# Optimization experiments

Hardware: AMD Instinct MI355X
Metric: run time of the kernel (lower is better)

## Reference

```python
import jax, jax.numpy as jnp
import numpy as np

N, E, D, SD = 50000, 800000, 64, 7

def _lin_init(key, fan_in, shape):
    b = 1.0 / np.sqrt(fan_in)
    return jax.random.uniform(key, shape, minval=-b, maxval=b, dtype=jnp.float32)

def setup_inputs() -> dict:
    key = jax.random.key(0)
    ks = jax.random.split(key, 16)
    edge_index = jax.random.randint(ks[0], (2, E), 0, N, dtype=jnp.int64)
    h = jax.random.normal(ks[1], (N, D), dtype=jnp.float32)
    return {
        "edge_index": edge_index,
        "h": h,
        "W_att": _lin_init(ks[2], D, (D, D)),        # stored [in,out]
        "phi_att_w": _lin_init(ks[3], D, (D, D)),
        "phi_att_b": _lin_init(ks[4], D, (D,)),
        "W_p": _lin_init(ks[5], D, (D, D)),
        "W_pp": _lin_init(ks[6], D, (D, D)),
        "f_def_w": _lin_init(ks[7], D, (D, 1)),
        "f_def_b": _lin_init(ks[8], D, (1,)),
        "W_self_w": _lin_init(ks[9], D, (D, D)),
        "W_self_b": _lin_init(ks[10], D, (D,)),
        "W_A_w": _lin_init(ks[11], D, (D, D)),
        "W_A_b": _lin_init(ks[12], D, (D,)),
        "W_str_w": _lin_init(ks[13], SD - 1, (SD - 1, D)),
        "W_str_b": _lin_init(ks[14], SD - 1, (D,)),
        "ln_g": jnp.ones((D,), jnp.float32),
        "ln_b": jnp.zeros((D,), jnp.float32),
    }

def reference(edge_index, h, W_att, phi_att_w, phi_att_b, W_p, W_pp,
              f_def_w, f_def_b, W_self_w, W_self_b, W_A_w, W_A_b,
              W_str_w, W_str_b, ln_g, ln_b):
    gamma, delta = 1.0, 0.5
    n = h.shape[0]
    src, tgt = edge_index[0], edge_index[1]
    H = h  # in_dim == hidden_dim -> embed is None
    s_feat = h[:, :SD - 1]                      # [N, 6]
    h_src, h_tgt = H[src], H[tgt]               # [E, D] gathers
    # attention-like scatter softmax over incoming edges of tgt
    score = jnp.sum(h_tgt * (h_src @ W_att), axis=-1) \
          + jnp.sum(s_feat[src] * s_feat[tgt], axis=-1)   # [E]
    alpha_num = jnp.exp(score)
    alpha_den = jax.ops.segment_sum(alpha_num, tgt, num_segments=n)
    alpha = alpha_num / (alpha_den[tgt] + 1e-9)
    # pairing / defense term (rev_src=tgt, rev_tgt=src => h_att=H[src], h_def=H[tgt])
    pair = jnp.sum((h_src @ W_p) * (h_tgt @ W_pp), axis=-1)  # [E]
    beta_num = jnp.exp(pair)
    beta_den = jax.ops.segment_sum(beta_num, src, num_segments=n)
    beta = beta_num / (beta_den[src] + 1e-9)
    psi = (h_tgt @ f_def_w)[:, 0] + f_def_b[0]                # [E]
    sum_term = jax.ops.segment_sum(beta * jnp.exp(-psi), src, num_segments=n)
    d = -jnp.log(sum_term + 1e-8)
    rho = jax.nn.sigmoid(gamma * (d - delta))                 # [N]
    rho_edge = rho[src]
    # message + scatter-sum aggregation
    msg = alpha[:, None] * (h_src @ phi_att_w + phi_att_b) * (1.0 - rho_edge)[:, None]
    m_att = jax.ops.segment_sum(msg, tgt, num_segments=n)     # [N, D]
    out = (H @ W_self_w + W_self_b) + (m_att @ W_A_w + W_A_b) \
        + (s_feat @ W_str_w + W_str_b)
    out = jax.nn.relu(out) + H                                # residual
    mu = jnp.mean(out, axis=-1, keepdims=True)
    var = jnp.mean((out - mu) ** 2, axis=-1, keepdims=True)
    out = (out - mu) / jnp.sqrt(var + 1e-5) * ln_g + ln_b     # LayerNorm
    return out
```

## Files before the change

kernel.cpp:

```cpp
#include <hip/hip_runtime.h>
#include <math.h>

#define D 64
#define NB 256
#define SCAN_NB 256

typedef _Float16 hf;
typedef _Float16 hf2 __attribute__((ext_vector_type(2)));

__device__ inline float fdot2f(hf2 a, hf2 b, float c) {
#if __has_builtin(__builtin_amdgcn_fdot2)
    return __builtin_amdgcn_fdot2(a, b, c, false);
#else
    return (float)a[0] * (float)b[0] + (float)a[1] * (float)b[1] + c;
#endif
}

__global__ __launch_bounds__(512) void node_pre_kernel(
    const float* __restrict__ h,
    const float* __restrict__ W_att,
    const float* __restrict__ W_p,
    const float* __restrict__ W_pp,
    const float* __restrict__ phi_w,
    const float* __restrict__ phi_b,
    const float* __restrict__ fdef_w,
    const float* __restrict__ fdef_b,
    hf* __restrict__ AW16,
    hf* __restrict__ P16,
    hf* __restrict__ PP16,
    float* __restrict__ enpsi,
    int nNodes)
{
    __shared__ hf2 sW2[4][32][D];
    __shared__ hf  hall[32][D];
    __shared__ float sPhib[D];
    __shared__ float sFdef[D];

    const int tid = threadIdx.x;
    const float* Wm[4] = { W_att, W_p, W_pp, phi_w };
    for (int idx = tid; idx < 4 * 32 * D; idx += 512) {
        const int m  = idx >> 11;
        const int k2 = (idx >> 6) & 31;
        const int j  = idx & 63;
        sW2[m][k2][j] = hf2{(hf)Wm[m][(2 * k2) * D + j], (hf)Wm[m][(2 * k2 + 1) * D + j]};
    }
    if (tid < D) { sPhib[tid] = phi_b[tid]; sFdef[tid] = fdef_w[tid]; }
    __syncthreads();
    const float fb = fdef_b[0];

    const int n0 = blockIdx.x * 32;
    {
        const int base = tid * 4;
        const int ln = base >> 6;
        const int col = base & 63;
        const int n = n0 + ln;
        float ps = 0.f;
        if (n < nNodes) {
            const float4 v = *(const float4*)(h + (size_t)n * D + col);
            hall[ln][col]     = (hf)v.x;
            hall[ln][col + 1] = (hf)v.y;
            hall[ln][col + 2] = (hf)v.z;
            hall[ln][col + 3] = (hf)v.w;
            ps = v.x * sFdef[col] + v.y * sFdef[col + 1]
               + v.z * sFdef[col + 2] + v.w * sFdef[col + 3];
        }
        #pragma unroll
        for (int off = 8; off >= 1; off >>= 1) ps += __shfl_xor(ps, off, 64);
        if ((tid & 15) == 0 && n < nNodes) enpsi[n] = __expf(-(ps + fb));
    }
    __syncthreads();

    const int g = tid >> 6;
    const int j = tid & 63;
    const int ln0 = 4 * g;

    float acc[4][4];
    #pragma unroll
    for (int m = 0; m < 4; ++m) {
        acc[m][0] = 0.f; acc[m][1] = 0.f; acc[m][2] = 0.f; acc[m][3] = sPhib[j];
    }
    const hf2* hr0 = (const hf2*)hall[ln0 + 0];
    const hf2* hr1 = (const hf2*)hall[ln0 + 1];
    const hf2* hr2 = (const hf2*)hall[ln0 + 2];
    const hf2* hr3 = (const hf2*)hall[ln0 + 3];

    #pragma unroll 8
    for (int k2 = 0; k2 < 32; ++k2) {
        const hf2 w0 = sW2[0][k2][j];
        const hf2 w1 = sW2[1][k2][j];
        const hf2 w2 = sW2[2][k2][j];
        const hf2 w3 = sW2[3][k2][j];
        const hf2 h0 = hr0[k2];
        const hf2 h1 = hr1[k2];
        const hf2 h2 = hr2[k2];
        const hf2 h3 = hr3[k2];
        acc[0][0] = fdot2f(w0, h0, acc[0][0]);
        acc[0][1] = fdot2f(w1, h0, acc[0][1]);
        acc[0][2] = fdot2f(w2, h0, acc[0][2]);
        acc[0][3] = fdot2f(w3, h0, acc[0][3]);
        acc[1][0] = fdot2f(w0, h1, acc[1][0]);
        acc[1][1] = fdot2f(w1, h1, acc[1][1]);
        acc[1][2] = fdot2f(w2, h1, acc[1][2]);
        acc[1][3] = fdot2f(w3, h1, acc[1][3]);
        acc[2][0] = fdot2f(w0, h2, acc[2][0]);
        acc[2][1] = fdot2f(w1, h2, acc[2][1]);
        acc[2][2] = fdot2f(w2, h2, acc[2][2]);
        acc[2][3] = fdot2f(w3, h2, acc[2][3]);
        acc[3][0] = fdot2f(w0, h3, acc[3][0]);
        acc[3][1] = fdot2f(w1, h3, acc[3][1]);
        acc[3][2] = fdot2f(w2, h3, acc[3][2]);
        acc[3][3] = fdot2f(w3, h3, acc[3][3]);
    }

    #pragma unroll
    for (int m = 0; m < 4; ++m) {
        const int n = n0 + ln0 + m;
        if (n < nNodes) {
            float a = acc[m][0];
            if (j < 6) a += (float)hall[ln0 + m][j];
            const size_t base = (size_t)n * D + j;
            *(hf2*)(AW16 + ((size_t)n << 7) + 2 * j) = hf2{(hf)a, (hf)acc[m][3]};
            P16[base]  = (hf)acc[m][1];
            PP16[base] = (hf)acc[m][2];
        }
    }
}

__global__ __launch_bounds__(256) void bucket_hist_kernel(
    const int* __restrict__ tgtI, const int* __restrict__ srcI,
    int* __restrict__ ghist_t, int* __restrict__ ghist_s,
    int nBkt, int nEdges)
{
    __shared__ int hist[2048];
    const int dir = blockIdx.x / NB;
    const int b = blockIdx.x % NB;
    const int* keys = dir ? srcI : tgtI;
    int* gh = dir ? ghist_s : ghist_t;
    const int tid = threadIdx.x;
    for (int d = tid; d < nBkt; d += 256) hist[d] = 0;
    __syncthreads();
    const int C = (nEdges + NB - 1) / NB;
    const int beg = b * C;
    const int end = min(beg + C, nEdges);
    for (int e = beg + tid; e < end; e += 256)
        atomicAdd(&hist[keys[e] >> 5], 1);
    __syncthreads();
    for (int d = tid; d < nBkt; d += 256)
        gh[(size_t)d * NB + b] = hist[d];
}

__global__ __launch_bounds__(256) void scan_partial_kernel(
    const int* __restrict__ in_t, const int* __restrict__ in_s,
    int* __restrict__ bsum, int L)
{
    const int pass = blockIdx.x >> 8;
    const int b = blockIdx.x & (SCAN_NB - 1);
    const int* in = pass ? in_s : in_t;
    const int C = (L + SCAN_NB - 1) / SCAN_NB;
    const int K = (C + 255) / 256;
    const int base = b * C;
    const int lim = min(base + C, L);
    const int tbeg = base + threadIdx.x * K;
    const int tend = min(tbeg + K, lim);
    int tsum = 0;
    for (int i = tbeg; i < tend; ++i) tsum += in[i];
    __shared__ int red[256];
    red[threadIdx.x] = tsum;
    __syncthreads();
    for (int off = 128; off >= 1; off >>= 1) {
        if (threadIdx.x < off) red[threadIdx.x] += red[threadIdx.x + off];
        __syncthreads();
    }
    if (threadIdx.x == 0) bsum[pass * SCAN_NB + b] = red[0];
}

__global__ __launch_bounds__(512) void scan_bsum_kernel(int* __restrict__ bsum)
{
    __shared__ int s[2 * SCAN_NB];
    const int tid = threadIdx.x;
    const int orig = bsum[tid];
    s[tid] = orig;
    __syncthreads();
    const int seg = tid & (SCAN_NB - 1);
    for (int off = 1; off < SCAN_NB; off <<= 1) {
        const int add = (seg >= off) ? s[tid - off] : 0;
        __syncthreads();
        s[tid] += add;
        __syncthreads();
    }
    bsum[tid] = s[tid] - orig;
}

__global__ __launch_bounds__(256) void scan_final_kernel(
    const int* __restrict__ in_t, const int* __restrict__ in_s,
    const int* __restrict__ bsum,
    int* __restrict__ gsc_t, int* __restrict__ gsc_s, int L)
{
    const int pass = blockIdx.x >> 8;
    const int b = blockIdx.x & (SCAN_NB - 1);
    const int* in = pass ? in_s : in_t;
    int* out = pass ? gsc_s : gsc_t;
    const int C = (L + SCAN_NB - 1) / SCAN_NB;
    const int K = (C + 255) / 256;
    const int base = b * C;
    const int lim = min(base + C, L);
    const int tbeg = base + threadIdx.x * K;
    const int tend = min(tbeg + K, lim);
    int tsum = 0;
    for (int i = tbeg; i < tend; ++i) tsum += in[i];
    __shared__ int s[256];
    s[threadIdx.x] = tsum;
    __syncthreads();
    for (int off = 1; off < 256; off <<= 1) {
        const int add = (threadIdx.x >= off) ? s[threadIdx.x - off] : 0;
        __syncthreads();
        s[threadIdx.x] += add;
        __syncthreads();
    }
    int run = s[threadIdx.x] - tsum + bsum[pass * SCAN_NB + b];
    for (int i = tbeg; i < tend; ++i) { out[i] = run; run += in[i]; }
}

__global__ __launch_bounds__(256) void bucket_scatter_kernel(
    const int* __restrict__ tgtI, const int* __restrict__ srcI,
    const int* __restrict__ gsc_t, const int* __restrict__ gsc_s,
    unsigned* __restrict__ ep_t, unsigned* __restrict__ ep_s,
    int nBkt, int nEdges)
{
    __shared__ int cursor[2048];
    const int dir = blockIdx.x / NB;
    const int b = blockIdx.x % NB;
    const int* keys = dir ? srcI : tgtI;
    const int* pays = dir ? tgtI : srcI;
    const int* gsc = dir ? gsc_s : gsc_t;
    unsigned* ep = dir ? ep_s : ep_t;
    const int tid = threadIdx.x;
    for (int d = tid; d < nBkt; d += 256) cursor[d] = gsc[(size_t)d * NB + b];
    __syncthreads();
    const int C = (nEdges + NB - 1) / NB;
    const int beg = b * C;
    const int end = min(beg + C, nEdges);
    for (int e = beg + tid; e < end; e += 256) {
        const unsigned k = (unsigned)keys[e];
        const unsigned p = (unsigned)pays[e];
        const int pos = atomicAdd(&cursor[k >> 5], 1);
        ep[pos] = (k << 16) | p;
    }
}

__global__ __launch_bounds__(256) void bucket_sort_kernel(
    const unsigned* __restrict__ ep_t, const unsigned* __restrict__ ep_s,
    const int* __restrict__ gsc_t, const int* __restrict__ gsc_s,
    int* __restrict__ src_sorted, int* __restrict__ tgt_sorted,
    int* __restrict__ rowstart_t, int* __restrict__ rowstart_s,
    int nBkt, int nNodes, int nEdges)
{
    __shared__ int hist[32], pref[32], cur[32];
    const int dir = (int)(blockIdx.x >= (unsigned)nBkt);
    const int b = blockIdx.x - dir * nBkt;
    const unsigned* ep = dir ? ep_s : ep_t;
    const int* gsc = dir ? gsc_s : gsc_t;
    int* out = dir ? tgt_sorted : src_sorted;
    int* rowstart = dir ? rowstart_s : rowstart_t;
    const int tid = threadIdx.x;

    if (blockIdx.x == 0 && tid == 0) rowstart_t[nNodes] = nEdges;
    if (blockIdx.x == (unsigned)nBkt && tid == 0) rowstart_s[nNodes] = nEdges;

    const int s = gsc[(size_t)b * NB];
    const int e = (b + 1 < nBkt) ? gsc[(size_t)(b + 1) * NB] : nEdges;
    const int size = e - s;

    if (tid < 32) hist[tid] = 0;
    __syncthreads();
    for (int i = tid; i < size; i += 256)
        atomicAdd(&hist[(ep[s + i] >> 16) & 31], 1);
    __syncthreads();
    if (tid == 0) {
        int r = 0;
        for (int k = 0; k < 32; ++k) { pref[k] = r; cur[k] = r; r += hist[k]; }
    }
    __syncthreads();
    if (tid < 32) {
        const int key = (b << 5) + tid;
        if (key < nNodes) rowstart[key] = s + pref[tid];
    }
    __syncthreads();
    for (int i = tid; i < size; i += 256) {
        const unsigned v = ep[s + i];
        const int pos = atomicAdd(&cur[(v >> 16) & 31], 1);
        out[s + pos] = (int)(v & 0xFFFFu);
    }
}

__global__ __launch_bounds__(256) void pass_src_kernel(
    const int* __restrict__ rowstart_s,
    const int* __restrict__ tgt_sorted,
    const hf* __restrict__ P16,
    const hf* __restrict__ PP16,
    const float* __restrict__ enpsi,
    hf* __restrict__ AW16,
    int nNodes)
{
    const int grp = threadIdx.x >> 4;
    const int l = threadIdx.x & 15;

    for (int n = blockIdx.x * 16 + grp; n < nNodes; n += gridDim.x * 16) {
        const int beg = rowstart_s[n];
        const int end = rowstart_s[n + 1];
        const float2 pr = ((const float2*)(P16 + (size_t)n * D))[l];
        const hf* pq = (const hf*)&pr;
        const float p0 = pq[0], p1 = pq[1], p2 = pq[2], p3 = pq[3];
        float bden = 0.f, ssum = 0.f;

        int k = beg;
        for (; k + 3 < end; k += 4) {
            const int tA = tgt_sorted[k],     tB = tgt_sorted[k + 1];
            const int tC = tgt_sorted[k + 2], tD = tgt_sorted[k + 3];
            const float2 rA = ((const float2*)(PP16 + (size_t)tA * D))[l];
            const float2 rB = ((const float2*)(PP16 + (size_t)tB * D))[l];
            const float2 rC = ((const float2*)(PP16 + (size_t)tC * D))[l];
            const float2 rD = ((const float2*)(PP16 + (size_t)tD * D))[l];
            const float eA = enpsi[tA], eB = enpsi[tB], eC = enpsi[tC], eD = enpsi[tD];
            const hf* qA = (const hf*)&rA;
            const hf* qB = (const hf*)&rB;
            const hf* qC = (const hf*)&rC;
            const hf* qD = (const hf*)&rD;
            float a2 = (float)qA[0] * p0 + (float)qA[1] * p1 + (float)qA[2] * p2 + (float)qA[3] * p3;
            float b2 = (float)qB[0] * p0 + (float)qB[1] * p1 + (float)qB[2] * p2 + (float)qB[3] * p3;
            float c2 = (float)qC[0] * p0 + (float)qC[1] * p1 + (float)qC[2] * p2 + (float)qC[3] * p3;
            float d2 = (float)qD[0] * p0 + (float)qD[1] * p1 + (float)qD[2] * p2 + (float)qD[3] * p3;
            #pragma unroll
            for (int off = 8; off >= 1; off >>= 1) {
                a2 += __shfl_xor(a2, off, 64);
                b2 += __shfl_xor(b2, off, 64);
                c2 += __shfl_xor(c2, off, 64);
                d2 += __shfl_xor(d2, off, 64);
            }
            const float bn0 = __expf(a2);
            const float bn1 = __expf(b2);
            const float bn2 = __expf(c2);
            const float bn3 = __expf(d2);
            bden += bn0 + bn1 + bn2 + bn3;
            ssum += bn0 * eA + bn1 * eB + bn2 * eC + bn3 * eD;
        }
        for (; k < end; ++k) {
            const int t = tgt_sorted[k];
            const float2 r = ((const float2*)(PP16 + (size_t)t * D))[l];
            const float et = enpsi[t];
            const hf* q = (const hf*)&r;
            float a2 = (float)q[0] * p0 + (float)q[1] * p1 + (float)q[2] * p2 + (float)q[3] * p3;
            #pragma unroll
            for (int off = 8; off >= 1; off >>= 1) a2 += __shfl_xor(a2, off, 64);
            const float bn = __expf(a2);
            bden += bn;
            ssum += bn * et;
        }
        const float st = ssum / (bden + 1e-9f);
        const float d = -logf(st + 1e-8f);
        const float w = 1.0f - 1.0f / (1.0f + __expf(-(d - 0.5f)));
        float4* rowp = (float4*)(AW16 + ((size_t)n << 7));
        float4 rv = rowp[l];
        hf* q = (hf*)&rv;
        q[1] = (hf)((float)q[1] * w);
        q[3] = (hf)((float)q[3] * w);
        q[5] = (hf)((float)q[5] * w);
        q[7] = (hf)((float)q[7] * w);
        rowp[l] = rv;
    }
}

__global__ __launch_bounds__(256) void pass_tgt_fused_kernel(
    const int* __restrict__ rowstart_t,
    const int* __restrict__ src_sorted,
    const float* __restrict__ h,
    const hf* __restrict__ AW16,
    hf* __restrict__ m16,
    int nNodes)
{
    const int grp = threadIdx.x >> 4;
    const int l = threadIdx.x & 15;

    for (int n = blockIdx.x * 16 + grp; n < nNodes; n += gridDim.x * 16) {
        const int beg = rowstart_t[n];
        const int end = rowstart_t[n + 1];
        const float4 htv = ((const float4*)(h + (size_t)n * D))[l];
        float aden = 0.f;
        float m0 = 0.f, m1 = 0.f, m2 = 0.f, m3 = 0.f;

        int k = beg;
        for (; k + 3 < end; k += 4) {
            const int sA = src_sorted[k],     sB = src_sorted[k + 1];
            const int sC = src_sorted[k + 2], sD = src_sorted[k + 3];
            const float4 rA = ((const float4*)(AW16 + ((size_t)sA << 7)))[l];
            const float4 rB = ((const float4*)(AW16 + ((size_t)sB << 7)))[l];
            const float4 rC = ((const float4*)(AW16 + ((size_t)sC << 7)))[l];
            const float4 rD = ((const float4*)(AW16 + ((size_t)sD << 7)))[l];
            const hf* qA = (const hf*)&rA;
            const hf* qB = (const hf*)&rB;
            const hf* qC = (const hf*)&rC;
            const hf* qD = (const hf*)&rD;
            float a1 = (float)qA[0] * htv.x + (float)qA[2] * htv.y + (float)qA[4] * htv.z + (float)qA[6] * htv.w;
            float b1 = (float)qB[0] * htv.x + (float)qB[2] * htv.y + (float)qB[4] * htv.z + (float)qB[6] * htv.w;
            float c1 = (float)qC[0] * htv.x + (float)qC[2] * htv.y + (float)qC[4] * htv.z + (float)qC[6] * htv.w;
            float d1 = (float)qD[0] * htv.x + (float)qD[2] * htv.y + (float)qD[4] * htv.z + (float)qD[6] * htv.w;
            #pragma unroll
            for (int off = 8; off >= 1; off >>= 1) {
                a1 += __shfl_xor(a1, off, 64);
                b1 += __shfl_xor(b1, off, 64);
                c1 += __shfl_xor(c1, off, 64);
                d1 += __shfl_xor(d1, off, 64);
            }
            const float an0 = __expf(a1);
            const float an1 = __expf(b1);
            const float an2 = __expf(c1);
            const float an3 = __expf(d1);
            aden += an0 + an1 + an2 + an3;
            m0 += an0 * (float)qA[1] + an1 * (float)qB[1] + an2 * (float)qC[1] + an3 * (float)qD[1];
            m1 += an0 * (float)qA[3] + an1 * (float)qB[3] + an2 * (float)qC[3] + an3 * (float)qD[3];
            m2 += an0 * (float)qA[5] + an1 * (float)qB[5] + an2 * (float)qC[5] + an3 * (float)qD[5];
            m3 += an0 * (float)qA[7] + an1 * (float)qB[7] + an2 * (float)qC[7] + an3 * (float)qD[7];
        }
        for (; k < end; ++k) {
            const int s = src_sorted[k];
            const float4 r = ((const float4*)(AW16 + ((size_t)s << 7)))[l];
            const hf* q = (const hf*)&r;
            float a1 = (float)q[0] * htv.x + (float)q[2] * htv.y + (float)q[4] * htv.z + (float)q[6] * htv.w;
            #pragma unroll
            for (int off = 8; off >= 1; off >>= 1) a1 += __shfl_xor(a1, off, 64);
            const float an = __expf(a1);
            aden += an;
            m0 += an * (float)q[1];
            m1 += an * (float)q[3];
            m2 += an * (float)q[5];
            m3 += an * (float)q[7];
        }

        const float idn = 1.0f / (aden + 1e-9f);
        hf o4[4];
        o4[0] = (hf)(m0 * idn);
        o4[1] = (hf)(m1 * idn);
        o4[2] = (hf)(m2 * idn);
        o4[3] = (hf)(m3 * idn);
        ((float2*)(m16 + (size_t)n * D))[l] = *(const float2*)o4;
    }
}

__global__ __launch_bounds__(512) void final_kernel(
    const float* __restrict__ h,
    const hf* __restrict__ m16,
    const float* __restrict__ W_self_w, const float* __restrict__ W_self_b,
    const float* __restrict__ W_A_w,    const float* __restrict__ W_A_b,
    const float* __restrict__ W_str_w,  const float* __restrict__ W_str_b,
    const float* __restrict__ ln_g,     const float* __restrict__ ln_b,
    float* __restrict__ out,
    int nNodes)
{
    __shared__ hf2 sWs2[32][D];
    __shared__ hf2 sWa2[32][D];
    __shared__ float sWstr[6 * D];
    __shared__ float sBias[D];
    __shared__ float sG[D], sB[D];
    __shared__ hf hall[32][D];
    __shared__ hf mall[32][D];

    const int tid = threadIdx.x;
    for (int idx = tid; idx < 32 * D; idx += 512) {
        const int k2 = idx >> 6, j = idx & 63;
        sWs2[k2][j] = hf2{(hf)W_self_w[(2 * k2) * D + j], (hf)W_self_w[(2 * k2 + 1) * D + j]};
        sWa2[k2][j] = hf2{(hf)W_A_w[(2 * k2) * D + j],    (hf)W_A_w[(2 * k2 + 1) * D + j]};
    }
    for (int i = tid; i < 6 * D; i += 512) sWstr[i] = W_str_w[i];
    if (tid < D) {
        sBias[tid] = W_self_b[tid] + W_A_b[tid] + W_str_b[tid];
        sG[tid] = ln_g[tid];
        sB[tid] = ln_b[tid];
    }

    const int n0 = blockIdx.x * 32;
    {
        const int base = tid * 4;
        const int ln = base >> 6;
        const int col = base & 63;
        const int n = n0 + ln;
        if (n < nNodes) {
            const float4 v = *(const float4*)(h + (size_t)n * D + col);
            hall[ln][col]     = (hf)v.x;
            hall[ln][col + 1] = (hf)v.y;
            hall[ln][col + 2] = (hf)v.z;
            hall[ln][col + 3] = (hf)v.w;
            *(uint2*)&mall[ln][col] = *(const uint2*)(m16 + (size_t)n * D + col);
        }
    }
    __syncthreads();

    const int g = tid >> 6, j = tid & 63;
    const int ln0 = 4 * g;

    float acc[4];
    #pragma unroll
    for (int m = 0; m < 4; ++m) acc[m] = sBias[j];

    const hf2* hr0 = (const hf2*)hall[ln0 + 0];
    const hf2* hr1 = (const hf2*)hall[ln0 + 1];
    const hf2* hr2 = (const hf2*)hall[ln0 + 2];
    const hf2* hr3 = (const hf2*)hall[ln0 + 3];
    const hf2* mr0 = (const hf2*)mall[ln0 + 0];
    const hf2* mr1 = (const hf2*)mall[ln0 + 1];
    const hf2* mr2 = (const hf2*)mall[ln0 + 2];
    const hf2* mr3 = (const hf2*)mall[ln0 + 3];

    #pragma unroll 8
    for (int k2 = 0; k2 < 32; ++k2) {
        const hf2 ws = sWs2[k2][j];
        const hf2 wa = sWa2[k2][j];
        acc[0] = fdot2f(ws, hr0[k2], acc[0]);
        acc[0] = fdot2f(wa, mr0[k2], acc[0]);
        acc[1] = fdot2f(ws, hr1[k2], acc[1]);
        acc[1] = fdot2f(wa, mr1[k2], acc[1]);
        acc[2] = fdot2f(ws, hr2[k2], acc[2]);
        acc[2] = fdot2f(wa, mr2[k2], acc[2]);
        acc[3] = fdot2f(ws, hr3[k2], acc[3]);
        acc[3] = fdot2f(wa, mr3[k2], acc[3]);
    }
    #pragma unroll
    for (int k = 0; k < 6; ++k) {
        const float w = sWstr[k * D + j];
        acc[0] += (float)hall[ln0 + 0][k] * w;
        acc[1] += (float)hall[ln0 + 1][k] * w;
        acc[2] += (float)hall[ln0 + 2][k] * w;
        acc[3] += (float)hall[ln0 + 3][k] * w;
    }

    float pre[4], mu[4], vv[4];
    #pragma unroll
    for (int m = 0; m < 4; ++m)
        pre[m] = fmaxf(acc[m], 0.f) + (float)hall[ln0 + m][j];

    #pragma unroll
    for (int m = 0; m < 4; ++m) mu[m] = pre[m];
    #pragma unroll
    for (int off = 32; off >= 1; off >>= 1) {
        #pragma unroll
        for (int m = 0; m < 4; ++m) mu[m] += __shfl_xor(mu[m], off, 64);
    }
    #pragma unroll
    for (int m = 0; m < 4; ++m) {
        mu[m] *= (1.0f / 64.0f);
        const float diff = pre[m] - mu[m];
        vv[m] = diff * diff;
    }
    #pragma unroll
    for (int off = 32; off >= 1; off >>= 1) {
        #pragma unroll
        for (int m = 0; m < 4; ++m) vv[m] += __shfl_xor(vv[m], off, 64);
    }
    #pragma unroll
    for (int m = 0; m < 4; ++m) {
        const int n = n0 + ln0 + m;
        if (n < nNodes) {
            const float diff = pre[m] - mu[m];
            out[(size_t)n * D + j] = diff * rsqrtf(vv[m] * (1.0f / 64.0f) + 1e-5f) * sG[j] + sB[j];
        }
    }
}

extern "C" void kernel_launch(void* const* d_in, const int* in_sizes, int n_in,
                              void* d_out, int out_size, void* d_ws, size_t ws_size,
                              hipStream_t stream) {
    const int* edge       = (const int*)d_in[0];
    const float* h        = (const float*)d_in[1];
    const float* W_att    = (const float*)d_in[2];
    const float* phi_w    = (const float*)d_in[3];
    const float* phi_b    = (const float*)d_in[4];
    const float* W_p      = (const float*)d_in[5];
    const float* W_pp     = (const float*)d_in[6];
    const float* fdef_w   = (const float*)d_in[7];
    const float* fdef_b   = (const float*)d_in[8];
    const float* W_self_w = (const float*)d_in[9];
    const float* W_self_b = (const float*)d_in[10];
    const float* W_A_w    = (const float*)d_in[11];
    const float* W_A_b    = (const float*)d_in[12];
    const float* W_str_w  = (const float*)d_in[13];
    const float* W_str_b  = (const float*)d_in[14];
    const float* ln_g     = (const float*)d_in[15];
    const float* ln_b     = (const float*)d_in[16];

    const int E = in_sizes[0] / 2;
    const int nNodes = in_sizes[1] / D;
    const int* srcI = edge;
    const int* tgtI = edge + E;
    const int nBkt = (nNodes + 31) / 32;
    const int L = nBkt * NB;
    const int nbNode = (nNodes + 31) / 32;

    char* ws = (char*)d_ws;
    size_t off = 0;
    auto alloc = [&](size_t bytes) { char* p = ws + off; off = (off + bytes + 255) & ~(size_t)255; return p; };

    hf*       AW16      = (hf*)      alloc((size_t)nNodes * 2 * D * 2);
    hf*       P16       = (hf*)      alloc((size_t)nNodes * D * 2);
    hf*       PP16      = (hf*)      alloc((size_t)nNodes * D * 2);
    hf*       m16       = (hf*)      alloc((size_t)nNodes * D * 2);
    float*    enpsi     = (float*)   alloc((size_t)nNodes * 4);
    int*      ghist_t   = (int*)     alloc((size_t)L * 4);
    int*      ghist_s   = (int*)     alloc((size_t)L * 4);
    int*      gsc_t     = (int*)     alloc((size_t)L * 4);
    int*      gsc_s     = (int*)     alloc((size_t)L * 4);
    unsigned* ep_t      = (unsigned*)alloc((size_t)E * 4);
    unsigned* ep_s      = (unsigned*)alloc((size_t)E * 4);
    int*      src_sorted= (int*)     alloc((size_t)E * 4);
    int*      tgt_sorted= (int*)     alloc((size_t)E * 4);
    int*      rowstart_t= (int*)     alloc(((size_t)nNodes + 1) * 4);
    int*      rowstart_s= (int*)     alloc(((size_t)nNodes + 1) * 4);
    int*      bsum      = (int*)     alloc((size_t)2 * SCAN_NB * 4);

    node_pre_kernel<<<nbNode, 512, 0, stream>>>(
        h, W_att, W_p, W_pp, phi_w, phi_b, fdef_w, fdef_b,
        AW16, P16, PP16, enpsi, nNodes);

    bucket_hist_kernel<<<2 * NB, 256, 0, stream>>>(
        tgtI, srcI, ghist_t, ghist_s, nBkt, E);

    scan_partial_kernel<<<2 * SCAN_NB, 256, 0, stream>>>(ghist_t, ghist_s, bsum, L);
    scan_bsum_kernel<<<1, 2 * SCAN_NB, 0, stream>>>(bsum);
    scan_final_kernel<<<2 * SCAN_NB, 256, 0, stream>>>(
        ghist_t, ghist_s, bsum, gsc_t, gsc_s, L);

    bucket_scatter_kernel<<<2 * NB, 256, 0, stream>>>(
        tgtI, srcI, gsc_t, gsc_s, ep_t, ep_s, nBkt, E);

    bucket_sort_kernel<<<2 * nBkt, 256, 0, stream>>>(
        ep_t, ep_s, gsc_t, gsc_s, src_sorted, tgt_sorted,
        rowstart_t, rowstart_s, nBkt, nNodes, E);

    pass_src_kernel<<<2048, 256, 0, stream>>>(
        rowstart_s, tgt_sorted, P16, PP16, enpsi, AW16, nNodes);

    pass_tgt_fused_kernel<<<2048, 256, 0, stream>>>(
        rowstart_t, src_sorted, h, AW16, m16, nNodes);

    final_kernel<<<nbNode, 512, 0, stream>>>(
        h, m16, W_self_w, W_self_b, W_A_w, W_A_b,
        W_str_w, W_str_b, ln_g, ln_b, (float*)d_out, nNodes);
}
```

Before: 174.4 us.

## Co-schedule histogram with node precompute and tgt-sort with src pass; unroll gathers by 8

```diff
diff --git a/kernel.cpp b/kernel.cpp
--- a/kernel.cpp
+++ b/kernel.cpp
@@ -4,6 +4,7 @@
 #define D 64
 #define NB 256
 #define SCAN_NB 256
+#define PS_NB 2048
 
 typedef _Float16 hf;
 typedef _Float16 hf2 __attribute__((ext_vector_type(2)));
@@ -16,7 +17,7 @@
 #endif
 }
 
-__global__ __launch_bounds__(512) void node_pre_kernel(
+__global__ __launch_bounds__(512) void node_pre_hist_kernel(
     const float* __restrict__ h,
     const float* __restrict__ W_att,
     const float* __restrict__ W_p,
@@ -25,18 +26,41 @@
     const float* __restrict__ phi_b,
     const float* __restrict__ fdef_w,
     const float* __restrict__ fdef_b,
+    const int* __restrict__ tgtI, const int* __restrict__ srcI,
+    int* __restrict__ ghist_t, int* __restrict__ ghist_s,
     hf* __restrict__ AW16,
     hf* __restrict__ P16,
     hf* __restrict__ PP16,
     float* __restrict__ enpsi,
-    int nNodes)
+    int nNodes, int nbNode, int nBkt, int nEdges)
 {
     __shared__ hf2 sW2[4][32][D];
     __shared__ hf  hall[32][D];
     __shared__ float sPhib[D];
     __shared__ float sFdef[D];
+    __shared__ int hist[2048];
 
     const int tid = threadIdx.x;
+
+    if (blockIdx.x >= nbNode) {
+        const int hb = blockIdx.x - nbNode;
+        const int dir = hb / NB;
+        const int b = hb % NB;
+        const int* keys = dir ? srcI : tgtI;
+        int* gh = dir ? ghist_s : ghist_t;
+        for (int d = tid; d < nBkt; d += 512) hist[d] = 0;
+        __syncthreads();
+        const int C = (nEdges + NB - 1) / NB;
+        const int beg = b * C;
+        const int end = min(beg + C, nEdges);
+        for (int e = beg + tid; e < end; e += 512)
+            atomicAdd(&hist[keys[e] >> 5], 1);
+        __syncthreads();
+        for (int d = tid; d < nBkt; d += 512)
+            gh[(size_t)d * NB + b] = hist[d];
+        return;
+    }
+
     const float* Wm[4] = { W_att, W_p, W_pp, phi_w };
     for (int idx = tid; idx < 4 * 32 * D; idx += 512) {
         const int m  = idx >> 11;
@@ -126,29 +150,6 @@
     }
 }
 
-__global__ __launch_bounds__(256) void bucket_hist_kernel(
-    const int* __restrict__ tgtI, const int* __restrict__ srcI,
-    int* __restrict__ ghist_t, int* __restrict__ ghist_s,
-    int nBkt, int nEdges)
-{
-    __shared__ int hist[2048];
-    const int dir = blockIdx.x / NB;
-    const int b = blockIdx.x % NB;
-    const int* keys = dir ? srcI : tgtI;
-    int* gh = dir ? ghist_s : ghist_t;
-    const int tid = threadIdx.x;
-    for (int d = tid; d < nBkt; d += 256) hist[d] = 0;
-    __syncthreads();
-    const int C = (nEdges + NB - 1) / NB;
-    const int beg = b * C;
-    const int end = min(beg + C, nEdges);
-    for (int e = beg + tid; e < end; e += 256)
-        atomicAdd(&hist[keys[e] >> 5], 1);
-    __syncthreads();
-    for (int d = tid; d < nBkt; d += 256)
-        gh[(size_t)d * NB + b] = hist[d];
-}
-
 __global__ __launch_bounds__(256) void scan_partial_kernel(
     const int* __restrict__ in_t, const int* __restrict__ in_s,
     int* __restrict__ bsum, int L)
@@ -248,24 +249,13 @@
     }
 }
 
-__global__ __launch_bounds__(256) void bucket_sort_kernel(
-    const unsigned* __restrict__ ep_t, const unsigned* __restrict__ ep_s,
-    const int* __restrict__ gsc_t, const int* __restrict__ gsc_s,
-    int* __restrict__ src_sorted, int* __restrict__ tgt_sorted,
-    int* __restrict__ rowstart_t, int* __restrict__ rowstart_s,
-    int nBkt, int nNodes, int nEdges)
-{
-    __shared__ int hist[32], pref[32], cur[32];
-    const int dir = (int)(blockIdx.x >= (unsigned)nBkt);
-    const int b = blockIdx.x - dir * nBkt;
-    const unsigned* ep = dir ? ep_s : ep_t;
-    const int* gsc = dir ? gsc_s : gsc_t;
-    int* out = dir ? tgt_sorted : src_sorted;
-    int* rowstart = dir ? rowstart_s : rowstart_t;
-    const int tid = threadIdx.x;
-
-    if (blockIdx.x == 0 && tid == 0) rowstart_t[nNodes] = nEdges;
-    if (blockIdx.x == (unsigned)nBkt && tid == 0) rowstart_s[nNodes] = nEdges;
+__device__ inline void bucket_sort_body(
+    const unsigned* __restrict__ ep, const int* __restrict__ gsc,
+    int* __restrict__ out, int* __restrict__ rowstart,
+    int b, int nBkt, int nNodes, int nEdges,
+    int* hist, int* pref, int* cur, int tid)
+{
+    if (b == 0 && tid == 0) rowstart[nNodes] = nEdges;
 
     const int s = gsc[(size_t)b * NB];
     const int e = (b + 1 < nBkt) ? gsc[(size_t)(b + 1) * NB] : nEdges;
@@ -293,19 +283,40 @@
     }
 }
 
-__global__ __launch_bounds__(256) void pass_src_kernel(
+__global__ __launch_bounds__(256) void bucket_sort_s_kernel(
+    const unsigned* __restrict__ ep_s, const int* __restrict__ gsc_s,
+    int* __restrict__ tgt_sorted, int* __restrict__ rowstart_s,
+    int nBkt, int nNodes, int nEdges)
+{
+    __shared__ int hist[32], pref[32], cur[32];
+    bucket_sort_body(ep_s, gsc_s, tgt_sorted, rowstart_s,
+                     blockIdx.x, nBkt, nNodes, nEdges, hist, pref, cur, threadIdx.x);
+}
+
+__global__ __launch_bounds__(256) void pass_src_sortT_kernel(
     const int* __restrict__ rowstart_s,
     const int* __restrict__ tgt_sorted,
     const hf* __restrict__ P16,
     const hf* __restrict__ PP16,
     const float* __restrict__ enpsi,
     hf* __restrict__ AW16,
-    int nNodes)
-{
-    const int grp = threadIdx.x >> 4;
-    const int l = threadIdx.x & 15;
-
-    for (int n = blockIdx.x * 16 + grp; n < nNodes; n += gridDim.x * 16) {
+    const unsigned* __restrict__ ep_t, const int* __restrict__ gsc_t,
+    int* __restrict__ src_sorted, int* __restrict__ rowstart_t,
+    int nBkt, int nNodes, int nEdges)
+{
+    __shared__ int hist[32], pref[32], cur[32];
+    const int tid = threadIdx.x;
+
+    if (blockIdx.x >= PS_NB) {
+        bucket_sort_body(ep_t, gsc_t, src_sorted, rowstart_t,
+                         blockIdx.x - PS_NB, nBkt, nNodes, nEdges, hist, pref, cur, tid);
+        return;
+    }
+
+    const int grp = tid >> 4;
+    const int l = tid & 15;
+
+    for (int n = blockIdx.x * 16 + grp; n < nNodes; n += PS_NB * 16) {
         const int beg = rowstart_s[n];
         const int end = rowstart_s[n + 1];
         const float2 pr = ((const float2*)(P16 + (size_t)n * D))[l];
@@ -314,35 +325,57 @@
         float bden = 0.f, ssum = 0.f;
 
         int k = beg;
+        for (; k + 7 < end; k += 8) {
+            int tv[8]; float2 rv[8]; float ev[8];
+            #pragma unroll
+            for (int u = 0; u < 8; ++u) tv[u] = tgt_sorted[k + u];
+            #pragma unroll
+            for (int u = 0; u < 8; ++u) rv[u] = ((const float2*)(PP16 + (size_t)tv[u] * D))[l];
+            #pragma unroll
+            for (int u = 0; u < 8; ++u) ev[u] = enpsi[tv[u]];
+            float sc[8];
+            #pragma unroll
+            for (int u = 0; u < 8; ++u) {
+                const hf* q = (const hf*)&rv[u];
+                sc[u] = (float)q[0] * p0 + (float)q[1] * p1 + (float)q[2] * p2 + (float)q[3] * p3;
+            }
+            #pragma unroll
+            for (int off = 8; off >= 1; off >>= 1) {
+                #pragma unroll
+                for (int u = 0; u < 8; ++u) sc[u] += __shfl_xor(sc[u], off, 64);
+            }
+            #pragma unroll
+            for (int u = 0; u < 8; ++u) {
+                const float bn = __expf(sc[u]);
+                bden += bn;
+                ssum += bn * ev[u];
+            }
+        }
         for (; k + 3 < end; k += 4) {
-            const int tA = tgt_sorted[k],     tB = tgt_sorted[k + 1];
-            const int tC = tgt_sorted[k + 2], tD = tgt_sorted[k + 3];
-            const float2 rA = ((const float2*)(PP16 + (size_t)tA * D))[l];
-            const float2 rB = ((const float2*)(PP16 + (size_t)tB * D))[l];
-            const float2 rC = ((const float2*)(PP16 + (size_t)tC * D))[l];
-            const float2 rD = ((const float2*)(PP16 + (size_t)tD * D))[l];
-            const float eA = enpsi[tA], eB = enpsi[tB], eC = enpsi[tC], eD = enpsi[tD];
-            const hf* qA = (const hf*)&rA;
-            const hf* qB = (const hf*)&rB;
-            const hf* qC = (const hf*)&rC;
-            const hf* qD = (const hf*)&rD;
-            float a2 = (float)qA[0] * p0 + (float)qA[1] * p1 + (float)qA[2] * p2 + (float)qA[3] * p3;
-            float b2 = (float)qB[0] * p0 + (float)qB[1] * p1 + (float)qB[2] * p2 + (float)qB[3] * p3;
-            float c2 = (float)qC[0] * p0 + (float)qC[1] * p1 + (float)qC[2] * p2 + (float)qC[3] * p3;
-            float d2 = (float)qD[0] * p0 + (float)qD[1] * p1 + (float)qD[2] * p2 + (float)qD[3] * p3;
+            int tv[4]; float2 rv[4]; float ev[4];
+            #pragma unroll
+            for (int u = 0; u < 4; ++u) tv[u] = tgt_sorted[k + u];
+            #pragma unroll
+            for (int u = 0; u < 4; ++u) rv[u] = ((const float2*)(PP16 + (size_t)tv[u] * D))[l];
+            #pragma unroll
+            for (int u = 0; u < 4; ++u) ev[u] = enpsi[tv[u]];
+            float sc[4];
+            #pragma unroll
+            for (int u = 0; u < 4; ++u) {
+                const hf* q = (const hf*)&rv[u];
+                sc[u] = (float)q[0] * p0 + (float)q[1] * p1 + (float)q[2] * p2 + (float)q[3] * p3;
+            }
             #pragma unroll
             for (int off = 8; off >= 1; off >>= 1) {
-                a2 += __shfl_xor(a2, off, 64);
-                b2 += __shfl_xor(b2, off, 64);
-                c2 += __shfl_xor(c2, off, 64);
-                d2 += __shfl_xor(d2, off, 64);
-            }
-            const float bn0 = __expf(a2);
-            const float bn1 = __expf(b2);
-            const float bn2 = __expf(c2);
-            const float bn3 = __expf(d2);
-            bden += bn0 + bn1 + bn2 + bn3;
-            ssum += bn0 * eA + bn1 * eB + bn2 * eC + bn3 * eD;
+                #pragma unroll
+                for (int u = 0; u < 4; ++u) sc[u] += __shfl_xor(sc[u], off, 64);
+            }
+            #pragma unroll
+            for (int u = 0; u < 4; ++u) {
+                const float bn = __expf(sc[u]);
+                bden += bn;
+                ssum += bn * ev[u];
+            }
         }
         for (; k < end; ++k) {
             const int t = tgt_sorted[k];
@@ -389,43 +422,70 @@
         float m0 = 0.f, m1 = 0.f, m2 = 0.f, m3 = 0.f;
 
         int k = beg;
+        for (; k + 7 < end; k += 8) {
+            int sv[8]; float4 rv[8];
+            #pragma unroll
+            for (int u = 0; u < 8; ++u) sv[u] = src_sorted[k + u];
+            #pragma unroll
+            for (int u = 0; u < 8; ++u) rv[u] = ((const float4*)(AW16 + ((size_t)sv[u] << 7)))[l];
+            float sc[8];
+            #pragma unroll
+            for (int u = 0; u < 8; ++u) {
+                const hf* q = (const hf*)&rv[u];
+                sc[u] = (float)q[0] * htv.x + (float)q[2] * htv.y
+                      + (float)q[4] * htv.z + (float)q[6] * htv.w;
+            }
+            #pragma unroll
+            for (int off = 8; off >= 1; off >>= 1) {
+                #pragma unroll
+                for (int u = 0; u < 8; ++u) sc[u] += __shfl_xor(sc[u], off, 64);
+            }
+            #pragma unroll
+            for (int u = 0; u < 8; ++u) {
+                const float an = __expf(sc[u]);
+                aden += an;
+                const hf* q = (const hf*)&rv[u];
+                m0 += an * (float)q[1];
+                m1 += an * (float)q[3];
+                m2 += an * (float)q[5];
+                m3 += an * (float)q[7];
+            }
+        }
         for (; k + 3 < end; k += 4) {
-            const int sA = src_sorted[k],     sB = src_sorted[k + 1];
-            const int sC = src_sorted[k + 2], sD = src_sorted[k + 3];
-            const float4 rA = ((const float4*)(AW16 + ((size_t)sA << 7)))[l];
-            const float4 rB = ((const float4*)(AW16 + ((size_t)sB << 7)))[l];
-            const float4 rC = ((const float4*)(AW16 + ((size_t)sC << 7)))[l];
-            const float4 rD = ((const float4*)(AW16 + ((size_t)sD << 7)))[l];
-            const hf* qA = (const hf*)&rA;
-            const hf* qB = (const hf*)&rB;
-            const hf* qC = (const hf*)&rC;
-            const hf* qD = (const hf*)&rD;
-            float a1 = (float)qA[0] * htv.x + (float)qA[2] * htv.y + (float)qA[4] * htv.z + (float)qA[6] * htv.w;
-            float b1 = (float)qB[0] * htv.x + (float)qB[2] * htv.y + (float)qB[4] * htv.z + (float)qB[6] * htv.w;
-            float c1 = (float)qC[0] * htv.x + (float)qC[2] * htv.y + (float)qC[4] * htv.z + (float)qC[6] * htv.w;
-            float d1 = (float)qD[0] * htv.x + (float)qD[2] * htv.y + (float)qD[4] * htv.z + (float)qD[6] * htv.w;
+            int sv[4]; float4 rv[4];
+            #pragma unroll
+            for (int u = 0; u < 4; ++u) sv[u] = src_sorted[k + u];
+            #pragma unroll
+            for (int u = 0; u < 4; ++u) rv[u] = ((const float4*)(AW16 + ((size_t)sv[u] << 7)))[l];
+            float sc[4];
+            #pragma unroll
+            for (int u = 0; u < 4; ++u) {
+                const hf* q = (const hf*)&rv[u];
+                sc[u] = (float)q[0] * htv.x + (float)q[2] * htv.y
+                      + (float)q[4] * htv.z + (float)q[6] * htv.w;
+            }
             #pragma unroll
             for (int off = 8; off >= 1; off >>= 1) {
-                a1 += __shfl_xor(a1, off, 64);
-                b1 += __shfl_xor(b1, off, 64);
-                c1 += __shfl_xor(c1, off, 64);
-                d1 += __shfl_xor(d1, off, 64);
-            }
-            const float an0 = __expf(a1);
-            const float an1 = __expf(b1);
-            const float an2 = __expf(c1);
-            const float an3 = __expf(d1);
-            aden += an0 + an1 + an2 + an3;
-            m0 += an0 * (float)qA[1] + an1 * (float)qB[1] + an2 * (float)qC[1] + an3 * (float)qD[1];
-            m1 += an0 * (float)qA[3] + an1 * (float)qB[3] + an2 * (float)qC[3] + an3 * (float)qD[3];
-            m2 += an0 * (float)qA[5] + an1 * (float)qB[5] + an2 * (float)qC[5] + an3 * (float)qD[5];
-            m3 += an0 * (float)qA[7] + an1 * (float)qB[7] + an2 * (float)qC[7] + an3 * (float)qD[7];
+                #pragma unroll
+                for (int u = 0; u < 4; ++u) sc[u] += __shfl_xor(sc[u], off, 64);
+            }
+            #pragma unroll
+            for (int u = 0; u < 4; ++u) {
+                const float an = __expf(sc[u]);
+                aden += an;
+                const hf* q = (const hf*)&rv[u];
+                m0 += an * (float)q[1];
+                m1 += an * (float)q[3];
+                m2 += an * (float)q[5];
+                m3 += an * (float)q[7];
+            }
         }
         for (; k < end; ++k) {
             const int s = src_sorted[k];
             const float4 r = ((const float4*)(AW16 + ((size_t)s << 7)))[l];
             const hf* q = (const hf*)&r;
-            float a1 = (float)q[0] * htv.x + (float)q[2] * htv.y + (float)q[4] * htv.z + (float)q[6] * htv.w;
+            float a1 = (float)q[0] * htv.x + (float)q[2] * htv.y
+                     + (float)q[4] * htv.z + (float)q[6] * htv.w;
             #pragma unroll
             for (int off = 8; off >= 1; off >>= 1) a1 += __shfl_xor(a1, off, 64);
             const float an = __expf(a1);
@@ -615,12 +675,10 @@
     int*      rowstart_s= (int*)     alloc(((size_t)nNodes + 1) * 4);
     int*      bsum      = (int*)     alloc((size_t)2 * SCAN_NB * 4);
 
-    node_pre_kernel<<<nbNode, 512, 0, stream>>>(
+    node_pre_hist_kernel<<<nbNode + 2 * NB, 512, 0, stream>>>(
         h, W_att, W_p, W_pp, phi_w, phi_b, fdef_w, fdef_b,
-        AW16, P16, PP16, enpsi, nNodes);
-
-    bucket_hist_kernel<<<2 * NB, 256, 0, stream>>>(
-        tgtI, srcI, ghist_t, ghist_s, nBkt, E);
+        tgtI, srcI, ghist_t, ghist_s,
+        AW16, P16, PP16, enpsi, nNodes, nbNode, nBkt, E);
 
     scan_partial_kernel<<<2 * SCAN_NB, 256, 0, stream>>>(ghist_t, ghist_s, bsum, L);
     scan_bsum_kernel<<<1, 2 * SCAN_NB, 0, stream>>>(bsum);
@@ -630,12 +688,12 @@
     bucket_scatter_kernel<<<2 * NB, 256, 0, stream>>>(
         tgtI, srcI, gsc_t, gsc_s, ep_t, ep_s, nBkt, E);
 
-    bucket_sort_kernel<<<2 * nBkt, 256, 0, stream>>>(
-        ep_t, ep_s, gsc_t, gsc_s, src_sorted, tgt_sorted,
-        rowstart_t, rowstart_s, nBkt, nNodes, E);
-
-    pass_src_kernel<<<2048, 256, 0, stream>>>(
-        rowstart_s, tgt_sorted, P16, PP16, enpsi, AW16, nNodes);
+    bucket_sort_s_kernel<<<nBkt, 256, 0, stream>>>(
+        ep_s, gsc_s, tgt_sorted, rowstart_s, nBkt, nNodes, E);
+
+    pass_src_sortT_kernel<<<PS_NB + nBkt, 256, 0, stream>>>(
+        rowstart_s, tgt_sorted, P16, PP16, enpsi, AW16,
+        ep_t, gsc_t, src_sorted, rowstart_t, nBkt, nNodes, E);
 
     pass_tgt_fused_kernel<<<2048, 256, 0, stream>>>(
         rowstart_t, src_sorted, h, AW16, m16, nNodes);
```

Measured after the change: 167.4 us. -4.0%, faster.
